# Performance work log

Measured on AMD Instinct MI355X. Metric: run time of the kernel, lower is better.

The kernel has to match this reference:

```python
import jax, jax.numpy as jnp
import numpy as np

EPS = 1e-8


def _conv1(x, w):
    # x: [C,H,W], w: [O,C,k,k] -> [O,H,W] (SAME padding, stride 1)
    return jax.lax.conv_general_dilated(
        x[None], w, window_strides=(1, 1), padding='SAME',
        dimension_numbers=('NCHW', 'OIHW', 'NCHW'))[0]


def setup_inputs() -> dict:
    key = jax.random.key(0)
    k1, k2, k3, k4 = jax.random.split(key, 4)
    B, C, O, K, S, H, W = 8, 512, 512, 3, 512, 64, 64
    inp = jax.random.normal(k1, (B, C, H, W), dtype=jnp.float32)
    style = jax.random.normal(k2, (B, S), dtype=jnp.float32)
    weight = jax.random.normal(k3, (1, O, C, K, K), dtype=jnp.float32)  # conv weight
    mod_weight = jax.random.normal(k4, (C, S), dtype=jnp.float32)      # EqualLinear weight
    mod_bias = jnp.ones((C,), dtype=jnp.float32)                        # bias filled with 1.0
    return {"input": inp, "style": style, "weight": weight,
            "mod_weight": mod_weight, "mod_bias": mod_bias}


def reference(input, style, weight, mod_weight, mod_bias) -> jnp.ndarray:
    B, C, H, W = input.shape
    _, O, _, K, _ = weight.shape
    fan_in = C * K * K
    scale = 1.0 / np.sqrt(fan_in)
    lin_scale = 1.0 / np.sqrt(mod_weight.shape[1])

    # EqualLinear modulation: [B, C]
    s = style @ (mod_weight * lin_scale).T + mod_bias

    # Modulate + demodulate per-sample weights: [B, O, C, K, K]
    w = scale * weight * s[:, None, :, None, None]
    demod = jax.lax.rsqrt(jnp.sum(w * w, axis=(2, 3, 4)) + EPS)  # [B, O]
    w = w * demod[:, :, None, None, None]

    # Grouped conv with groups=B == per-sample conv, vmapped over batch
    out = jax.vmap(_conv1)(input, w)  # [B, O, H, W]
    return out
```

## Files before the change

kernel.cpp:

```cpp
#include <hip/hip_runtime.h>

typedef unsigned short u16;
typedef __bf16 bf16_t;
typedef bf16_t bf16x8 __attribute__((ext_vector_type(8)));
typedef float floatx4 __attribute__((ext_vector_type(4)));

static constexpr float kScale = 0.014731391274719741f;
static constexpr float kScale2 = 2.1701388888888894e-4f;
static constexpr float kLinScale = 0.044194173824159216f;

__device__ __forceinline__ u16 f2bf(float f) {
  unsigned u = __float_as_uint(f);
  u += 0x7FFFu + ((u >> 16) & 1u);
  return (u16)(u >> 16);
}

#define GLD16(g, l)                                                        \
  __builtin_amdgcn_global_load_lds(                                        \
      (const __attribute__((address_space(1))) unsigned int*)(g),          \
      (__attribute__((address_space(3))) unsigned int*)(l), 16, 0, 0)

__global__ __launch_bounds__(256) void k_prep1(const float* __restrict__ style,
                                               const float* __restrict__ modw,
                                               const float* __restrict__ modb,
                                               const float* __restrict__ weight,
                                               float* __restrict__ s_buf,
                                               float* __restrict__ ssq) {
  int tid = threadIdx.x;
  if (blockIdx.x < 1024) {
    int lane = tid & 63, wv = tid >> 6;
    int idx = blockIdx.x * 4 + wv;
    int b = idx >> 9, c = idx & 511;
    const float* st = style + b * 512;
    const float* mw = modw + (size_t)c * 512;
    float s = 0.f;
#pragma unroll
    for (int i = 0; i < 8; ++i) s += st[lane + i * 64] * mw[lane + i * 64];
#pragma unroll
    for (int off = 32; off; off >>= 1) s += __shfl_xor(s, off);
    if (lane == 0) s_buf[idx] = s * kLinScale + modb[c];
  } else {
    int e = (blockIdx.x - 1024) * 256 + tid;
    const float* wp = weight + (size_t)e * 9;
    float ss = 0.f;
#pragma unroll
    for (int t = 0; t < 9; ++t) ss += wp[t] * wp[t];
    ssq[e] = ss;
  }
}

__global__ __launch_bounds__(256) void k_demod2(const float* __restrict__ ssq,
                                                const float* __restrict__ s_buf,
                                                float* __restrict__ demod_buf) {
  int tid = threadIdx.x, lane = tid & 63, wv = tid >> 6;
  int idx = blockIdx.x * 4 + wv;
  int b = idx >> 9, o = idx & 511;
  const float* sq = ssq + (size_t)o * 512;
  const float* srow = s_buf + b * 512;
  float ss = 0.f;
#pragma unroll
  for (int i = 0; i < 8; ++i) {
    float s = srow[lane + i * 64];
    ss += sq[lane + i * 64] * s * s;
  }
#pragma unroll
  for (int off = 32; off; off >>= 1) ss += __shfl_xor(ss, off);
  if (lane == 0) demod_buf[idx] = rsqrtf(ss * kScale2 + 1e-8f);
}

__global__ __launch_bounds__(256) void k_transpose(const float* __restrict__ in,
                                                   const float* __restrict__ s_buf,
                                                   unsigned* __restrict__ in_t32) {
  __shared__ u16 tile[64 * 65];
  int tid = threadIdx.x;
  int c0 = blockIdx.x * 64, y = blockIdx.y, b = blockIdx.z;
  const float* src = in + ((size_t)(b * 512 + c0) * 4096) + y * 64;
  const float* srow = s_buf + b * 512 + c0;
#pragma unroll
  for (int it = 0; it < 16; ++it) {
    int idx = it * 256 + tid;
    int cl = idx >> 6, x = idx & 63;
    tile[cl * 65 + x] = f2bf(src[(size_t)cl * 4096 + x] * srow[cl]);
  }
  __syncthreads();
  unsigned* dst = in_t32 + ((size_t)(b * 64 + y) * 64) * 256 + (c0 >> 1);
#pragma unroll
  for (int it = 0; it < 8; ++it) {
    int flat = it * 256 + tid;
    int cl2 = flat & 31, x = flat >> 5;
    unsigned lo = tile[(2 * cl2) * 65 + x];
    unsigned hi = tile[(2 * cl2 + 1) * 65 + x];
    dst[(size_t)x * 256 + cl2] = lo | (hi << 16);
  }
}

__global__ __launch_bounds__(256) void k_wfrag(const float* __restrict__ weight,
                                               unsigned* __restrict__ wt32) {
  __shared__ u16 tiles[9][512];
  int tid = threadIdx.x;
  int ct = blockIdx.x, ot = blockIdx.y;
  int o0 = ot * 16, c0 = ct * 32;
#pragma unroll
  for (int i = 0; i < 18; ++i) {
    int flat = i * 256 + tid;
    int t9 = flat / 9;
    int tap = flat - t9 * 9;
    int o_l = t9 >> 5, c_l = t9 & 31;
    float w = weight[((size_t)(o0 + o_l) * 512 + c0 + c_l) * 9 + tap];
    int pos = ((o_l + ((c_l >> 3) << 4)) << 3) + (c_l & 7);
    tiles[tap][pos] = f2bf(w * kScale);
  }
  __syncthreads();
  const unsigned* tl = (const unsigned*)tiles;
#pragma unroll
  for (int tap = 0; tap < 9; ++tap)
    wt32[(size_t)((tap * 16 + ct) * 32 + ot) * 256 + tid] = tl[tap * 256 + tid];
}

__global__ __launch_bounds__(256) void k_conv(const u16* __restrict__ in_t,
                                              const u16* __restrict__ w_t,
                                              const float* __restrict__ demod_buf,
                                              float* __restrict__ out) {
  __shared__ char smem[40960];
  char* As = smem;
  char* Bs = smem + 24576;
  const int tid = threadIdx.x;
  const int lane = tid & 63;
  const int wv = tid >> 6;
  const int wm = wv >> 1, wn = wv & 1;
  const int quad = lane >> 4, m16 = lane & 15;
  const int nt = blockIdx.x, mt = blockIdx.y, b = blockIdx.z;
  const int y0 = nt * 2;

  floatx4 acc[4][4];
#pragma unroll
  for (int i = 0; i < 4; ++i)
#pragma unroll
    for (int j = 0; j < 4; ++j) acc[i][j] = (floatx4){0.f, 0.f, 0.f, 0.f};

  for (int ct = 0; ct < 16; ++ct) {
    const int c0 = ct * 32;
#pragma unroll
    for (int r = 0; r < 4; ++r) {
      const int ci = r * 256 + tid;
      const int s = ci >> 2, qi = ci & 3;
      const int x = s & 63;
      const int y = y0 - 1 + r;
      const int qd = qi ^ (x & 3);
      char* lbase = Bs + (r * 4 + wv) * 1024;
      if ((unsigned)y < 64u) {
        const u16* g = in_t + (((size_t)(b * 64 + y) * 64 + x) * 512 + c0 + qd * 8);
        GLD16(g, lbase);
      } else {
        *(uint4*)(Bs + ci * 16) = make_uint4(0u, 0u, 0u, 0u);
      }
    }
    for (int dy = 0; dy < 3; ++dy) {
#pragma unroll
      for (int r6 = 0; r6 < 6; ++r6) {
        const int sec = r6 >> 1, half = r6 & 1;
        const int tap = dy * 3 + sec;
        const u16* g = w_t + ((size_t)(tap * 16 + ct) << 14) +
                       mt * 4096 + half * 2048 + wv * 512 + lane * 8;
        char* lbase = As + sec * 8192 + half * 4096 + wv * 1024;
        GLD16(g, lbase);
      }
      __syncthreads();
#pragma unroll
      for (int dx = 0; dx < 3; ++dx) {
        bf16x8 af[4];
#pragma unroll
        for (int ms = 0; ms < 4; ++ms)
          af[ms] = *(const bf16x8*)(As + dx * 8192 + (wm * 4 + ms) * 1024 + lane * 16);
#pragma unroll
        for (int ns = 0; ns < 4; ++ns) {
          const int nl = wn * 64 + ns * 16 + m16;
          const int ly = nl >> 6, lx = nl & 63;
          const int sx = lx + dx - 1;
          bf16x8 bv;
          if ((unsigned)sx < 64u) {
            const int s = (ly + dy) * 64 + sx;
            bv = *(const bf16x8*)(Bs + s * 64 + ((quad ^ (sx & 3)) << 4));
          } else {
#pragma unroll
            for (int j = 0; j < 8; ++j) bv[j] = (bf16_t)0.f;
          }
#pragma unroll
          for (int ms = 0; ms < 4; ++ms)
            acc[ms][ns] =
                __builtin_amdgcn_mfma_f32_16x16x32_bf16(af[ms], bv, acc[ms][ns], 0, 0, 0);
        }
      }
      __syncthreads();
    }
  }
  const int ob = mt * 128 + wm * 64;
  const int nb = nt * 128 + wn * 64;
#pragma unroll
  for (int ms = 0; ms < 4; ++ms)
#pragma unroll
    for (int ns = 0; ns < 4; ++ns) {
      const int n = nb + ns * 16 + m16;
#pragma unroll
      for (int r = 0; r < 4; ++r) {
        const int o = ob + ms * 16 + quad * 4 + r;
        float dm = demod_buf[b * 512 + o];
        out[((size_t)(b * 512 + o) << 12) + n] = acc[ms][ns][r] * dm;
      }
    }
}

extern "C" void kernel_launch(void* const* d_in, const int* in_sizes, int n_in,
                              void* d_out, int out_size, void* d_ws, size_t ws_size,
                              hipStream_t stream) {
  const float* input = (const float*)d_in[0];
  const float* style = (const float*)d_in[1];
  const float* weight = (const float*)d_in[2];
  const float* modw = (const float*)d_in[3];
  const float* modb = (const float*)d_in[4];
  float* out = (float*)d_out;
  char* ws = (char*)d_ws;
  float* s_buf = (float*)ws;
  float* demod_buf = (float*)(ws + 16384);
  float* ssq = (float*)(ws + 32768);
  u16* in_t = (u16*)(ws + 32768 + 1048576);
  u16* w_t = (u16*)(ws + 32768 + 1048576 + 33554432);

  k_prep1<<<dim3(2048), dim3(256), 0, stream>>>(style, modw, modb, weight, s_buf, ssq);
  k_demod2<<<dim3(1024), dim3(256), 0, stream>>>(ssq, s_buf, demod_buf);
  k_transpose<<<dim3(8, 64, 8), dim3(256), 0, stream>>>(input, s_buf, (unsigned*)in_t);
  k_wfrag<<<dim3(16, 32), dim3(256), 0, stream>>>(weight, (unsigned*)w_t);
  k_conv<<<dim3(32, 4, 8), dim3(256), 0, stream>>>(in_t, w_t, demod_buf, out);
}
```

Measured before the change: 267.9 us.

## Double-buffer weight tiles and prefetch input tiles through registers in conv

Double-buffers the A (weight) LDS tiles so the next tap-row's weights load while the current one runs on MFMA. The next channel tile's input halo is prefetched into registers during the last dy step and written to LDS afterwards. MFMA sections also raise wave priority via s_setprio. The aim is to hide global-load latency behind compute and remove one barrier stall per step. In exchange LDS grows to 64KB, which may cut occupancy, and the register prefetch adds VGPR pressure and an extra barrier per channel tile.

```diff
diff --git a/kernel.cpp b/kernel.cpp
--- a/kernel.cpp
+++ b/kernel.cpp
@@ -121,9 +121,9 @@
                                               const u16* __restrict__ w_t,
                                               const float* __restrict__ demod_buf,
                                               float* __restrict__ out) {
-  __shared__ char smem[40960];
-  char* As = smem;
-  char* Bs = smem + 24576;
+  __shared__ char smem[65536];
+  char* As0 = smem;
+  char* Bs = smem + 49152;
   const int tid = threadIdx.x;
   const int lane = tid & 63;
   const int wv = tid >> 6;
@@ -138,62 +138,115 @@
 #pragma unroll
     for (int j = 0; j < 4; ++j) acc[i][j] = (floatx4){0.f, 0.f, 0.f, 0.f};
 
+#define STAGE_A(ct_, dy_, Abuf)                                              \
+  {                                                                          \
+    _Pragma("unroll") for (int r6 = 0; r6 < 6; ++r6) {                       \
+      const int sec = r6 >> 1, half = r6 & 1;                                \
+      const int tap = (dy_)*3 + sec;                                         \
+      const u16* g = w_t + ((size_t)(tap * 16 + (ct_)) << 14) +              \
+                     mt * 4096 + half * 2048 + wv * 512 + lane * 8;          \
+      char* lbase = (Abuf) + sec * 8192 + half * 4096 + wv * 1024;           \
+      GLD16(g, lbase);                                                       \
+    }                                                                        \
+  }
+
+#define STAGE_B_LDS(ct_)                                                     \
+  {                                                                          \
+    const int c0s = (ct_)*32;                                                \
+    _Pragma("unroll") for (int r = 0; r < 4; ++r) {                          \
+      const int ci = r * 256 + tid;                                          \
+      const int s = ci >> 2, qi = ci & 3;                                    \
+      const int x = s & 63;                                                  \
+      const int y = y0 - 1 + r;                                              \
+      const int qd = qi ^ (x & 3);                                           \
+      char* lbase = Bs + (r * 4 + wv) * 1024;                                \
+      if ((unsigned)y < 64u) {                                               \
+        const u16* g =                                                       \
+            in_t + (((size_t)(b * 64 + y) * 64 + x) * 512 + c0s + qd * 8);   \
+        GLD16(g, lbase);                                                     \
+      } else {                                                               \
+        *(uint4*)(Bs + ci * 16) = make_uint4(0u, 0u, 0u, 0u);                \
+      }                                                                      \
+    }                                                                        \
+  }
+
+#define COMPUTE(dy_, Abase)                                                  \
+  {                                                                          \
+    __builtin_amdgcn_s_setprio(1);                                           \
+    _Pragma("unroll") for (int dx = 0; dx < 3; ++dx) {                       \
+      bf16x8 af[4];                                                          \
+      _Pragma("unroll") for (int ms = 0; ms < 4; ++ms)                       \
+        af[ms] = *(const bf16x8*)((Abase) + dx * 8192 +                      \
+                                  (wm * 4 + ms) * 1024 + lane * 16);         \
+      _Pragma("unroll") for (int ns = 0; ns < 4; ++ns) {                     \
+        const int nl = wn * 64 + ns * 16 + m16;                              \
+        const int ly = nl >> 6, lx = nl & 63;                                \
+        const int sx = lx + dx - 1;                                          \
+        bf16x8 bv;                                                           \
+        if ((unsigned)sx < 64u) {                                            \
+          const int s = (ly + (dy_)) * 64 + sx;                              \
+          bv = *(const bf16x8*)(Bs + s * 64 + ((quad ^ (sx & 3)) << 4));     \
+        } else {                                                             \
+          _Pragma("unroll") for (int j = 0; j < 8; ++j) bv[j] = (bf16_t)0.f; \
+        }                                                                    \
+        _Pragma("unroll") for (int ms = 0; ms < 4; ++ms)                     \
+          acc[ms][ns] = __builtin_amdgcn_mfma_f32_16x16x32_bf16(             \
+              af[ms], bv, acc[ms][ns], 0, 0, 0);                             \
+      }                                                                      \
+    }                                                                        \
+    __builtin_amdgcn_s_setprio(0);                                           \
+  }
+
+  STAGE_B_LDS(0);
+  STAGE_A(0, 0, As0);
+  __syncthreads();
+
+  int pa = 0;
   for (int ct = 0; ct < 16; ++ct) {
-    const int c0 = ct * 32;
-#pragma unroll
-    for (int r = 0; r < 4; ++r) {
-      const int ci = r * 256 + tid;
-      const int s = ci >> 2, qi = ci & 3;
-      const int x = s & 63;
-      const int y = y0 - 1 + r;
-      const int qd = qi ^ (x & 3);
-      char* lbase = Bs + (r * 4 + wv) * 1024;
-      if ((unsigned)y < 64u) {
-        const u16* g = in_t + (((size_t)(b * 64 + y) * 64 + x) * 512 + c0 + qd * 8);
-        GLD16(g, lbase);
+#pragma unroll
+    for (int dy = 0; dy < 3; ++dy) {
+      char* Acur = As0 + pa * 24576;
+      char* Anxt = As0 + (pa ^ 1) * 24576;
+      if (dy < 2) {
+        STAGE_A(ct, dy + 1, Anxt);
+        COMPUTE(dy, Acur);
+        __syncthreads();
       } else {
-        *(uint4*)(Bs + ci * 16) = make_uint4(0u, 0u, 0u, 0u);
-      }
-    }
-    for (int dy = 0; dy < 3; ++dy) {
-#pragma unroll
-      for (int r6 = 0; r6 < 6; ++r6) {
-        const int sec = r6 >> 1, half = r6 & 1;
-        const int tap = dy * 3 + sec;
-        const u16* g = w_t + ((size_t)(tap * 16 + ct) << 14) +
-                       mt * 4096 + half * 2048 + wv * 512 + lane * 8;
-        char* lbase = As + sec * 8192 + half * 4096 + wv * 1024;
-        GLD16(g, lbase);
-      }
-      __syncthreads();
-#pragma unroll
-      for (int dx = 0; dx < 3; ++dx) {
-        bf16x8 af[4];
-#pragma unroll
-        for (int ms = 0; ms < 4; ++ms)
-          af[ms] = *(const bf16x8*)(As + dx * 8192 + (wm * 4 + ms) * 1024 + lane * 16);
-#pragma unroll
-        for (int ns = 0; ns < 4; ++ns) {
-          const int nl = wn * 64 + ns * 16 + m16;
-          const int ly = nl >> 6, lx = nl & 63;
-          const int sx = lx + dx - 1;
-          bf16x8 bv;
-          if ((unsigned)sx < 64u) {
-            const int s = (ly + dy) * 64 + sx;
-            bv = *(const bf16x8*)(Bs + s * 64 + ((quad ^ (sx & 3)) << 4));
-          } else {
-#pragma unroll
-            for (int j = 0; j < 8; ++j) bv[j] = (bf16_t)0.f;
+        uint4 breg[4];
+        if (ct < 15) {
+          const int c0n = (ct + 1) * 32;
+#pragma unroll
+          for (int r = 0; r < 4; ++r) {
+            const int ci = r * 256 + tid;
+            const int s = ci >> 2, qi = ci & 3;
+            const int x = s & 63;
+            const int y = y0 - 1 + r;
+            const int qd = qi ^ (x & 3);
+            if ((unsigned)y < 64u)
+              breg[r] = *(const uint4*)(in_t + (((size_t)(b * 64 + y) * 64 + x) * 512 +
+                                                c0n + qd * 8));
+            else
+              breg[r] = make_uint4(0u, 0u, 0u, 0u);
           }
-#pragma unroll
-          for (int ms = 0; ms < 4; ++ms)
-            acc[ms][ns] =
-                __builtin_amdgcn_mfma_f32_16x16x32_bf16(af[ms], bv, acc[ms][ns], 0, 0, 0);
+          STAGE_A(ct + 1, 0, Anxt);
+        }
+        COMPUTE(2, Acur);
+        __syncthreads();
+        if (ct < 15) {
+#pragma unroll
+          for (int r = 0; r < 4; ++r)
+            *(uint4*)(Bs + (size_t)(r * 256 + tid) * 16) = breg[r];
+          __syncthreads();
         }
       }
-      __syncthreads();
+      pa ^= 1;
     }
   }
+
+#undef STAGE_A
+#undef STAGE_B_LDS
+#undef COMPUTE
+
   const int ob = mt * 128 + wm * 64;
   const int nb = nt * 128 + wn * 64;
 #pragma unroll
```

After: 258.7 us. 3.5% less time.

## Double-buffer input tiles and stream weight fragments directly into registers

Applied to the files above, without the earlier changes.

The conv kernel stops staging weight fragments in LDS. Each wave now loads its A fragments straight from global memory into registers, prefetching the next tap one step ahead. The input tile is double-buffered in LDS so the next channel chunk loads while the current one is computed, which cuts barriers from two per dy to one per chunk. It also adds s_setprio around the MFMA bursts, sets launch bounds for 4 blocks per CU, and remaps block indices so batch varies fastest. This trades LDS traffic and barrier stalls for more register pressure and global/L2 load latency on the A fragments.

```diff
diff --git a/kernel.cpp b/kernel.cpp
--- a/kernel.cpp
+++ b/kernel.cpp
@@ -117,19 +117,21 @@
     wt32[(size_t)((tap * 16 + ct) * 32 + ot) * 256 + tid] = tl[tap * 256 + tid];
 }
 
-__global__ __launch_bounds__(256) void k_conv(const u16* __restrict__ in_t,
-                                              const u16* __restrict__ w_t,
-                                              const float* __restrict__ demod_buf,
-                                              float* __restrict__ out) {
-  __shared__ char smem[40960];
-  char* As = smem;
-  char* Bs = smem + 24576;
+__global__ __launch_bounds__(256, 4) void k_conv(const u16* __restrict__ in_t,
+                                                 const u16* __restrict__ w_t,
+                                                 const float* __restrict__ demod_buf,
+                                                 float* __restrict__ out) {
+  __shared__ char smem[32768];
   const int tid = threadIdx.x;
   const int lane = tid & 63;
   const int wv = tid >> 6;
   const int wm = wv >> 1, wn = wv & 1;
   const int quad = lane >> 4, m16 = lane & 15;
-  const int nt = blockIdx.x, mt = blockIdx.y, b = blockIdx.z;
+  const int lin = blockIdx.x + 32 * blockIdx.y + 128 * blockIdx.z;
+  const int b = lin & 7;
+  const int r_ = lin >> 3;
+  const int nt = r_ & 31;
+  const int mt = r_ >> 5;
   const int y0 = nt * 2;
 
   floatx4 acc[4][4];
@@ -138,62 +140,79 @@
 #pragma unroll
     for (int j = 0; j < 4; ++j) acc[i][j] = (floatx4){0.f, 0.f, 0.f, 0.f};
 
+  const u16* abase = w_t + mt * 4096 + wm * 2048 + lane * 8;
+
+#define STAGE_B(ct_, Bbuf)                                                   \
+  {                                                                          \
+    const int c0s = (ct_)*32;                                                \
+    _Pragma("unroll") for (int r = 0; r < 4; ++r) {                          \
+      const int ci = r * 256 + tid;                                          \
+      const int s = ci >> 2, qi = ci & 3;                                    \
+      const int x = s & 63;                                                  \
+      const int y = y0 - 1 + r;                                              \
+      const int qd = qi ^ (x & 3);                                           \
+      char* lbase = (Bbuf) + (r * 4 + wv) * 1024;                            \
+      if ((unsigned)y < 64u) {                                               \
+        const u16* g =                                                       \
+            in_t + (((size_t)(b * 64 + y) * 64 + x) * 512 + c0s + qd * 8);   \
+        GLD16(g, lbase);                                                     \
+      } else {                                                               \
+        *(uint4*)((Bbuf) + ci * 16) = make_uint4(0u, 0u, 0u, 0u);            \
+      }                                                                      \
+    }                                                                        \
+  }
+
+  STAGE_B(0, smem);
+  bf16x8 afc[4];
+#pragma unroll
+  for (int ms = 0; ms < 4; ++ms)
+    afc[ms] = *(const bf16x8*)(abase + ms * 512);
+  __syncthreads();
+
+  int cur = 0;
   for (int ct = 0; ct < 16; ++ct) {
-    const int c0 = ct * 32;
-#pragma unroll
-    for (int r = 0; r < 4; ++r) {
-      const int ci = r * 256 + tid;
-      const int s = ci >> 2, qi = ci & 3;
-      const int x = s & 63;
-      const int y = y0 - 1 + r;
-      const int qd = qi ^ (x & 3);
-      char* lbase = Bs + (r * 4 + wv) * 1024;
-      if ((unsigned)y < 64u) {
-        const u16* g = in_t + (((size_t)(b * 64 + y) * 64 + x) * 512 + c0 + qd * 8);
-        GLD16(g, lbase);
-      } else {
-        *(uint4*)(Bs + ci * 16) = make_uint4(0u, 0u, 0u, 0u);
+    char* Bs = smem + cur * 16384;
+    char* Bn = smem + (cur ^ 1) * 16384;
+    if (ct < 15) STAGE_B(ct + 1, Bn);
+#pragma unroll
+    for (int t = 0; t < 9; ++t) {
+      const int dy = t / 3, dx = t % 3;
+      const int tn = (t == 8) ? 0 : t + 1;
+      const int ctn = (t == 8) ? ((ct + 1) & 15) : ct;
+      const u16* apn = abase + ((size_t)(tn * 16 + ctn) << 14);
+      bf16x8 afn[4];
+#pragma unroll
+      for (int ms = 0; ms < 4; ++ms)
+        afn[ms] = *(const bf16x8*)(apn + ms * 512);
+      __builtin_amdgcn_s_setprio(1);
+#pragma unroll
+      for (int ns = 0; ns < 4; ++ns) {
+        const int nl = wn * 64 + ns * 16 + m16;
+        const int ly = nl >> 6, lx = nl & 63;
+        const int sx = lx + dx - 1;
+        bf16x8 bv;
+        if ((unsigned)sx < 64u) {
+          const int s = (ly + dy) * 64 + sx;
+          bv = *(const bf16x8*)(Bs + s * 64 + ((quad ^ (sx & 3)) << 4));
+        } else {
+#pragma unroll
+          for (int j = 0; j < 8; ++j) bv[j] = (bf16_t)0.f;
+        }
+#pragma unroll
+        for (int ms = 0; ms < 4; ++ms)
+          acc[ms][ns] = __builtin_amdgcn_mfma_f32_16x16x32_bf16(
+              afc[ms], bv, acc[ms][ns], 0, 0, 0);
       }
+      __builtin_amdgcn_s_setprio(0);
+#pragma unroll
+      for (int ms = 0; ms < 4; ++ms) afc[ms] = afn[ms];
     }
-    for (int dy = 0; dy < 3; ++dy) {
-#pragma unroll
-      for (int r6 = 0; r6 < 6; ++r6) {
-        const int sec = r6 >> 1, half = r6 & 1;
-        const int tap = dy * 3 + sec;
-        const u16* g = w_t + ((size_t)(tap * 16 + ct) << 14) +
-                       mt * 4096 + half * 2048 + wv * 512 + lane * 8;
-        char* lbase = As + sec * 8192 + half * 4096 + wv * 1024;
-        GLD16(g, lbase);
-      }
-      __syncthreads();
-#pragma unroll
-      for (int dx = 0; dx < 3; ++dx) {
-        bf16x8 af[4];
-#pragma unroll
-        for (int ms = 0; ms < 4; ++ms)
-          af[ms] = *(const bf16x8*)(As + dx * 8192 + (wm * 4 + ms) * 1024 + lane * 16);
-#pragma unroll
-        for (int ns = 0; ns < 4; ++ns) {
-          const int nl = wn * 64 + ns * 16 + m16;
-          const int ly = nl >> 6, lx = nl & 63;
-          const int sx = lx + dx - 1;
-          bf16x8 bv;
-          if ((unsigned)sx < 64u) {
-            const int s = (ly + dy) * 64 + sx;
-            bv = *(const bf16x8*)(Bs + s * 64 + ((quad ^ (sx & 3)) << 4));
-          } else {
-#pragma unroll
-            for (int j = 0; j < 8; ++j) bv[j] = (bf16_t)0.f;
-          }
-#pragma unroll
-          for (int ms = 0; ms < 4; ++ms)
-            acc[ms][ns] =
-                __builtin_amdgcn_mfma_f32_16x16x32_bf16(af[ms], bv, acc[ms][ns], 0, 0, 0);
-        }
-      }
-      __syncthreads();
-    }
-  }
+    __syncthreads();
+    cur ^= 1;
+  }
+
+#undef STAGE_B
+
   const int ob = mt * 128 + wm * 64;
   const int nb = nt * 128 + wn * 64;
 #pragma unroll
```

New measurement: 450.4 us. 68.1% more time.

## Stream conv weights from global into registers and double-buffer input tile in LDS

Applied to the files above, without the earlier changes.

The conv main loop is restructured so weight fragments are loaded straight from global memory into registers one tap ahead, instead of being staged through LDS. The input halo tile is double-buffered in LDS with padded rows, so the next channel slice loads while the current one computes, with a single barrier per slice. The change also zero-fills the padding once up front, remaps block indices so batch varies fastest, raises MFMA priority and sets a 3-blocks-per-CU occupancy hint. It trades LDS traffic for more register pressure and relies on the L2 cache to serve weight reuse across blocks.

```diff
diff --git a/kernel.cpp b/kernel.cpp
--- a/kernel.cpp
+++ b/kernel.cpp
@@ -117,19 +117,21 @@
     wt32[(size_t)((tap * 16 + ct) * 32 + ot) * 256 + tid] = tl[tap * 256 + tid];
 }
 
-__global__ __launch_bounds__(256) void k_conv(const u16* __restrict__ in_t,
-                                              const u16* __restrict__ w_t,
-                                              const float* __restrict__ demod_buf,
-                                              float* __restrict__ out) {
-  __shared__ char smem[40960];
-  char* As = smem;
-  char* Bs = smem + 24576;
+__global__ __launch_bounds__(256, 3) void k_conv(const u16* __restrict__ in_t,
+                                                 const u16* __restrict__ w_t,
+                                                 const float* __restrict__ demod_buf,
+                                                 float* __restrict__ out) {
+  __shared__ char smem[33792];
   const int tid = threadIdx.x;
   const int lane = tid & 63;
   const int wv = tid >> 6;
   const int wm = wv >> 1, wn = wv & 1;
   const int quad = lane >> 4, m16 = lane & 15;
-  const int nt = blockIdx.x, mt = blockIdx.y, b = blockIdx.z;
+  const int lin = blockIdx.x + 32 * blockIdx.y + 128 * blockIdx.z;
+  const int b = lin & 7;
+  const int r_ = lin >> 3;
+  const int nt = r_ & 31;
+  const int mt = r_ >> 5;
   const int y0 = nt * 2;
 
   floatx4 acc[4][4];
@@ -138,62 +140,90 @@
 #pragma unroll
     for (int j = 0; j < 4; ++j) acc[i][j] = (floatx4){0.f, 0.f, 0.f, 0.f};
 
-  for (int ct = 0; ct < 16; ++ct) {
-    const int c0 = ct * 32;
-#pragma unroll
-    for (int r = 0; r < 4; ++r) {
-      const int ci = r * 256 + tid;
-      const int s = ci >> 2, qi = ci & 3;
-      const int x = s & 63;
-      const int y = y0 - 1 + r;
-      const int qd = qi ^ (x & 3);
-      char* lbase = Bs + (r * 4 + wv) * 1024;
-      if ((unsigned)y < 64u) {
-        const u16* g = in_t + (((size_t)(b * 64 + y) * 64 + x) * 512 + c0 + qd * 8);
-        GLD16(g, lbase);
-      } else {
-        *(uint4*)(Bs + ci * 16) = make_uint4(0u, 0u, 0u, 0u);
-      }
-    }
-    for (int dy = 0; dy < 3; ++dy) {
-#pragma unroll
-      for (int r6 = 0; r6 < 6; ++r6) {
-        const int sec = r6 >> 1, half = r6 & 1;
-        const int tap = dy * 3 + sec;
-        const u16* g = w_t + ((size_t)(tap * 16 + ct) << 14) +
-                       mt * 4096 + half * 2048 + wv * 512 + lane * 8;
-        char* lbase = As + sec * 8192 + half * 4096 + wv * 1024;
-        GLD16(g, lbase);
-      }
-      __syncthreads();
-#pragma unroll
-      for (int dx = 0; dx < 3; ++dx) {
-        bf16x8 af[4];
-#pragma unroll
-        for (int ms = 0; ms < 4; ++ms)
-          af[ms] = *(const bf16x8*)(As + dx * 8192 + (wm * 4 + ms) * 1024 + lane * 16);
-#pragma unroll
-        for (int ns = 0; ns < 4; ++ns) {
-          const int nl = wn * 64 + ns * 16 + m16;
-          const int ly = nl >> 6, lx = nl & 63;
-          const int sx = lx + dx - 1;
-          bf16x8 bv;
-          if ((unsigned)sx < 64u) {
-            const int s = (ly + dy) * 64 + sx;
-            bv = *(const bf16x8*)(Bs + s * 64 + ((quad ^ (sx & 3)) << 4));
-          } else {
-#pragma unroll
-            for (int j = 0; j < 8; ++j) bv[j] = (bf16_t)0.f;
-          }
-#pragma unroll
-          for (int ms = 0; ms < 4; ++ms)
-            acc[ms][ns] =
-                __builtin_amdgcn_mfma_f32_16x16x32_bf16(af[ms], bv, acc[ms][ns], 0, 0, 0);
-        }
-      }
-      __syncthreads();
-    }
-  }
+  const u16* abase = w_t + mt * 4096 + wm * 2048 + lane * 8;
+
+  const int xs = tid >> 2, qs = tid & 3;
+  const int qd = qs ^ ((xs >> 1) & 3);
+  const u16* gB[4];
+  bool rok[4];
+#pragma unroll
+  for (int r = 0; r < 4; ++r) {
+    int y = y0 - 1 + r;
+    rok[r] = (unsigned)y < 64u;
+    gB[r] = in_t + (((size_t)(b * 64 + (rok[r] ? y : 0)) * 64 + xs) * 512 + qd * 8);
+  }
+
+  char* bA[3];
+#pragma unroll
+  for (int dx = 0; dx < 3; ++dx) {
+    const int sx0 = m16 + dx - 1;
+    bA[dx] = smem + wn * 4224 + (sx0 + 1) * 64 + ((quad ^ ((sx0 >> 1) & 3)) << 4);
+  }
+
+  bf16x8 aR[2][4];
+  bf16x8 bv[2][4];
+
+#define LOAD_BV(si, bufimm, t_)                                              \
+  {                                                                          \
+    const int dy_ = (t_) / 3, dx_ = (t_) % 3;                                \
+    _Pragma("unroll") for (int ns = 0; ns < 4; ++ns)                         \
+      bv[si][ns] = *(const bf16x8*)(bA[dx_] + (bufimm) + dy_ * 4224 +        \
+                                    ns * 1024);                              \
+  }
+
+#define STAGE_B(bufimm)                                                      \
+  {                                                                          \
+    _Pragma("unroll") for (int r = 0; r < 4; ++r)                            \
+      if (rok[r]) GLD16(gB[r], smem + (bufimm) + r * 4224 + 64 + wv * 1024); \
+  }
+
+#define CT_BODY(ctv, par, CURIMM, NXTIMM)                                    \
+  {                                                                          \
+    LOAD_BV(par, CURIMM, 0);                                                 \
+    if ((ctv) + 1 < 16) {                                                    \
+      _Pragma("unroll") for (int r = 0; r < 4; ++r) gB[r] += 32;             \
+      STAGE_B(NXTIMM);                                                       \
+    }                                                                        \
+    _Pragma("unroll") for (int t = 0; t < 9; ++t) {                          \
+      const int icur = (t + (par)) & 1;                                      \
+      const int inxt = icur ^ 1;                                             \
+      const int tp = t < 8 ? t + 1 : 0;                                      \
+      const int ctp = t < 8 ? (ctv) : (ctv) + 1;                             \
+      const u16* ap = abase + ((size_t)(tp * 16 + ctp) << 14);               \
+      _Pragma("unroll") for (int ms = 0; ms < 4; ++ms)                       \
+        aR[inxt][ms] = *(const bf16x8*)(ap + ms * 512);                      \
+      if (t < 8) { LOAD_BV(inxt, CURIMM, t + 1); }                           \
+      __builtin_amdgcn_s_setprio(1);                                         \
+      _Pragma("unroll") for (int ns = 0; ns < 4; ++ns)                       \
+        _Pragma("unroll") for (int ms = 0; ms < 4; ++ms)                     \
+          acc[ms][ns] = __builtin_amdgcn_mfma_f32_16x16x32_bf16(             \
+              aR[icur][ms], bv[icur][ns], acc[ms][ns], 0, 0, 0);             \
+      __builtin_amdgcn_s_setprio(0);                                         \
+    }                                                                        \
+    asm volatile("s_waitcnt vmcnt(4)" ::: "memory");                         \
+    __builtin_amdgcn_s_barrier();                                            \
+  }
+
+  {
+    const uint4 z = make_uint4(0u, 0u, 0u, 0u);
+    for (int i = tid; i < 2112; i += 256) ((uint4*)smem)[i] = z;
+  }
+  __syncthreads();
+  STAGE_B(0);
+  __syncthreads();
+#pragma unroll
+  for (int ms = 0; ms < 4; ++ms)
+    aR[0][ms] = *(const bf16x8*)(abase + ms * 512);
+
+  for (int ct = 0; ct < 16; ct += 2) {
+    CT_BODY(ct, 0, 0, 16896);
+    CT_BODY(ct + 1, 1, 16896, 0);
+  }
+
+#undef LOAD_BV
+#undef STAGE_B
+#undef CT_BODY
+
   const int ob = mt * 128 + wm * 64;
   const int nb = nt * 128 + wn * 64;
 #pragma unroll
```

Measured after the change: 253.6 us. 1.06x faster.
